# Performance work log

Hardware: AMD Instinct MI355X
Metric: run time of the kernel (lower is better)

Reference implementation:

```python
import jax, jax.numpy as jnp
import numpy as np

HID = 1024
HEADS = 16
DH = HID // HEADS
SCALE = DH ** -0.5
L, B = 2048, 2


def setup_inputs() -> dict:
    key = jax.random.key(0)
    ks = jax.random.split(key, 16)
    inp = {
        "query": jax.random.normal(ks[0], (L, B, HID), jnp.float32),
        "key": jax.random.normal(ks[1], (L, B, HID), jnp.float32),
        "value": jax.random.normal(ks[2], (L, B, HID), jnp.float32),
        "mask": jax.random.randint(ks[3], (B, L), 0, 2).astype(bool),
    }
    # xavier-uniform linear weights (torch Linear stores [out, in]; y = x @ W.T + b)
    lim = (6.0 / (HID + HID)) ** 0.5
    for i, name in enumerate(["wq", "wk", "wv", "wfc"]):
        inp[name] = jax.random.uniform(ks[4 + i], (HID, HID), jnp.float32, -lim, lim)
    inp["bq"] = jnp.zeros((HID,), jnp.float32)
    inp["bk"] = jnp.zeros((HID,), jnp.float32)
    inp["bv"] = jnp.zeros((HID,), jnp.float32)
    inp["bfc"] = jnp.zeros((HID,), jnp.float32)
    inp["tao"] = jnp.full((HEADS,), 10.0, jnp.float32)
    return inp


def reference(query, key, value, mask, wq, bq, wk, bk, wv, bv, wfc, bfc, tao):
    # inputs arrive [L, B, D]; module transposes to [B, L, D]
    q = jnp.swapaxes(query, 0, 1)
    k = jnp.swapaxes(key, 0, 1)
    v = jnp.swapaxes(value, 0, 1)
    bsz, length, _ = q.shape

    def heads(x, w, b):
        y = x @ w.T + b                      # [B, L, D]
        return y.reshape(bsz, length, HEADS, DH).transpose(0, 2, 1, 3)  # [B, H, L, d]

    Q = heads(q, wq, bq)
    K = heads(k, wk, bk)
    V = heads(v, wv, bv)

    qk = jnp.einsum("bhqd,bhkd->bhqk", Q, K) * SCALE  # [B, H, L, L]

    # gaussian positional bias: -|i-j|^2/2 * tao_h^-4
    idx = jnp.arange(length, dtype=jnp.float32)
    dist = -0.5 * (idx[:, None] - idx[None, :]) ** 2          # [L, L]
    qk = qk + dist[None, None, :, :] * (tao ** -4)[None, :, None, None]

    qk = jnp.where(mask[:, None, None, :], -jnp.inf, qk)
    attn = jax.nn.softmax(qk, axis=-1)  # dropout is identity in eval mode

    x = jnp.einsum("bhqk,bhkd->bhqd", attn, V)            # [B, H, L, d]
    x = x.transpose(0, 2, 1, 3).reshape(bsz, length, HID)  # [B, L, D]
    x = x @ wfc.T + bfc
    return jnp.swapaxes(x, 0, 1)  # [L, B, D]
```

## Files before the change

### kernel.cpp

```cpp
#include <hip/hip_runtime.h>

#define LQ   2048
#define BQ   2
#define HID  1024
#define NH   16
#define DH   64
#define SCALE 0.125f
#define L2E  1.44269504088896f
#define C1   0.18033688011f
#define EXPOFF 23.0831206542f
#define MASKNEG (-1024.0f)

using short8  = __attribute__((ext_vector_type(8))) short;
using ushort8 = __attribute__((ext_vector_type(8))) unsigned short;
using f32x4   = __attribute__((ext_vector_type(4))) float;
typedef unsigned short u16;
typedef __attribute__((ext_vector_type(2))) __bf16 bf16x2;

__device__ inline u16 f2bf(float x) {
    unsigned int u = __float_as_uint(x);
    u = (u + 0x7fffu + ((u >> 16) & 1u)) >> 16;
    return (u16)u;
}

#if defined(__has_builtin)
#if __has_builtin(__builtin_amdgcn_cvt_pk_bf16_f32)
#define HAVE_PKBF 1
#endif
#if __has_builtin(__builtin_amdgcn_exp2f)
#define HAVE_EXP2 1
#endif
#endif

__device__ inline unsigned int pkbf(float a, float b) {
#ifdef HAVE_PKBF
    bf16x2 r = __builtin_amdgcn_cvt_pk_bf16_f32(a, b);
    return __builtin_bit_cast(unsigned int, r);
#else
    return (unsigned int)f2bf(a) | ((unsigned int)f2bf(b) << 16);
#endif
}

__device__ inline float fexp2(float x) {
#ifdef HAVE_EXP2
    return __builtin_amdgcn_exp2f(x);
#else
    return exp2f(x);
#endif
}

__device__ inline void gl_lds16(const void* g, void* l) {
    __builtin_amdgcn_global_load_lds(
        (const __attribute__((address_space(1))) void*)g,
        (__attribute__((address_space(3))) void*)l, 16, 0, 0);
}

__device__ inline void wvm8() { asm volatile("s_waitcnt vmcnt(8)" ::: "memory"); __builtin_amdgcn_sched_barrier(0); }
__device__ inline void wvm6() { asm volatile("s_waitcnt vmcnt(6)" ::: "memory"); __builtin_amdgcn_sched_barrier(0); }
__device__ inline void wvm0() { asm volatile("s_waitcnt vmcnt(0)" ::: "memory"); __builtin_amdgcn_sched_barrier(0); }
__device__ inline void wlg0() { asm volatile("s_waitcnt lgkmcnt(0)" ::: "memory"); __builtin_amdgcn_sched_barrier(0); }
__device__ inline void sbar() {
    __builtin_amdgcn_sched_barrier(0);
    __builtin_amdgcn_s_barrier();
    __builtin_amdgcn_sched_barrier(0);
}

struct CastArgs {
    const float* s[7];
    u16* d[7];
    int n[7];
    const unsigned char* mraw;
    float* mout;
    int mn;
};

__global__ __launch_bounds__(256) void castw(CastArgs a) {
    const int y = blockIdx.y;
    const int t = threadIdx.x;
    if (y == 7) {
        if (blockIdx.x != 0) return;
        __shared__ int cnt;
        if (t == 0) cnt = 0;
        __syncthreads();
        int local = 0;
        for (int i = t; i < a.mn; i += 256)
            if ((i & 3) && a.mraw[i]) local++;
        atomicAdd(&cnt, local);
        __syncthreads();
        bool isInt32 = (cnt == 0);
        const int* mi = (const int*)a.mraw;
        for (int i = t; i < a.mn; i += 256) {
            const bool m = isInt32 ? (mi[i] != 0) : (a.mraw[i] != 0);
            a.mout[i] = m ? (MASKNEG - EXPOFF) : (-EXPOFF);
        }
        return;
    }
    const float* s = a.s[y];
    u16* d = a.d[y];
    const int n4 = a.n[y] >> 2;
    for (int i = blockIdx.x * 256 + t; i < n4; i += gridDim.x * 256) {
        float4 v = *(const float4*)(s + (size_t)i * 4);
        uint2 p;
        p.x = pkbf(v.x, v.y);
        p.y = pkbf(v.z, v.w);
        *(uint2*)(d + (size_t)i * 4) = p;
    }
}

struct QkvArgs {
    const u16* A[3];
    const u16* W[3];
    const float* bias[3];
    u16* out[3];
};

__global__ __launch_bounds__(256) void gemm_qkv(QkvArgs ga) {
    __shared__ u16 As[2][128][64];
    __shared__ u16 Bs[2][128][64];

    const int z = blockIdx.z;
    const u16* A = ga.A[z];
    const u16* W = ga.W[z];
    const float* bias = ga.bias[z];
    u16* outp = ga.out[z];

    const int t = threadIdx.x;
    const int m0 = blockIdx.x * 128;
    const int n0 = blockIdx.y * 128;
    const int lane = t & 63;
    const int lane15 = lane & 15;
    const int quad = lane >> 4;
    const int w = t >> 6;
    const int wm = (w >> 1) * 64;
    const int wn = (w & 1) * 64;

    const int lrow = lane >> 3;
    const int ch = (lane & 7) ^ ((lane >> 3) & 7);
    const u16* aS = A + (size_t)(m0 + 32 * w + lrow) * HID + 8 * ch;
    const u16* bS = W + (size_t)(n0 + 32 * w + lrow) * HID + 8 * ch;

    const int s0 = (quad ^ (lane15 & 7)) * 8;
    const int s1 = ((4 + quad) ^ (lane15 & 7)) * 8;

    f32x4 acc[4][4];
#pragma unroll
    for (int i = 0; i < 4; i++)
#pragma unroll
        for (int j = 0; j < 4; j++) acc[i][j] = (f32x4){0,0,0,0};

#define QKV_STAGE(kt, buf)                                                          \
    {                                                                               \
        _Pragma("unroll")                                                           \
        for (int i = 0; i < 4; i++) {                                               \
            gl_lds16(aS + (size_t)(8 * i) * HID + 64 * (kt), &As[buf][32 * w + 8 * i][0]); \
            gl_lds16(bS + (size_t)(8 * i) * HID + 64 * (kt), &Bs[buf][32 * w + 8 * i][0]); \
        }                                                                           \
    }

    QKV_STAGE(0, 0);
    QKV_STAGE(1, 1);

    for (int kt = 0; kt < 16; ++kt) {
        if (kt < 15) wvm8(); else wvm0();
        sbar();

        const int pb = kt & 1;
        short8 af0[4], af1[4], bf0[4], bf1[4];
#pragma unroll
        for (int i = 0; i < 4; i++) {
            const u16* ar = &As[pb][wm + i * 16 + lane15][0];
            const u16* br = &Bs[pb][wn + i * 16 + lane15][0];
            af0[i] = *(const short8*)(ar + s0);
            af1[i] = *(const short8*)(ar + s1);
            bf0[i] = *(const short8*)(br + s0);
            bf1[i] = *(const short8*)(br + s1);
        }
        wlg0();
        sbar();
        if (kt + 2 < 16) QKV_STAGE(kt + 2, pb);

#pragma unroll
        for (int mi = 0; mi < 4; mi++)
#pragma unroll
            for (int ni = 0; ni < 4; ni++) {
                acc[mi][ni] = __builtin_amdgcn_mfma_f32_16x16x32_bf16(af0[mi], bf0[ni], acc[mi][ni], 0, 0, 0);
                acc[mi][ni] = __builtin_amdgcn_mfma_f32_16x16x32_bf16(af1[mi], bf1[ni], acc[mi][ni], 0, 0, 0);
            }
    }
#undef QKV_STAGE

#pragma unroll
    for (int mi = 0; mi < 4; mi++) {
#pragma unroll
        for (int ni = 0; ni < 4; ni++) {
            const int n = n0 + wn + ni * 16 + lane15;
            const float bv = bias[n];
            const int h = n >> 6, d = n & 63;
#pragma unroll
            for (int r = 0; r < 4; r++) {
                const int m = m0 + wm + mi * 16 + quad * 4 + r;
                const float c = acc[mi][ni][r] + bv;
                const int b = m & 1, l = m >> 1;
                if (z < 2) {
                    outp[(((size_t)(b * NH + h)) * LQ + l) * DH + d] = f2bf(c);
                } else {
                    outp[(((size_t)(b * NH + h)) * DH + d) * LQ + l] = f2bf(c);
                }
            }
        }
    }
}

__global__ __launch_bounds__(256) void gemm_fc(const u16* __restrict__ A,
                                               const u16* __restrict__ W,
                                               const float* __restrict__ bias,
                                               float* __restrict__ outp) {
    __shared__ u16 As[2][128][64];
    __shared__ u16 Bs[2][64][64];

    const int t = threadIdx.x;
    const int m0 = blockIdx.x * 128;
    const int n0 = blockIdx.y * 64;
    const int lane = t & 63;
    const int lane15 = lane & 15;
    const int quad = lane >> 4;
    const int w = t >> 6;
    const int wm = (w >> 1) * 64;
    const int wn = (w & 1) * 32;

    const int lrow = lane >> 3;
    const int ch = (lane & 7) ^ ((lane >> 3) & 7);
    const u16* aS = A + (size_t)(m0 + 32 * w + lrow) * HID + 8 * ch;
    const u16* bS = W + (size_t)(n0 + 16 * w + lrow) * HID + 8 * ch;

    const int s0 = (quad ^ (lane15 & 7)) * 8;
    const int s1 = ((4 + quad) ^ (lane15 & 7)) * 8;

    f32x4 acc[4][2];
#pragma unroll
    for (int i = 0; i < 4; i++)
#pragma unroll
        for (int j = 0; j < 2; j++) acc[i][j] = (f32x4){0,0,0,0};

#define FC_STAGE(kt, buf)                                                           \
    {                                                                               \
        _Pragma("unroll")                                                           \
        for (int i = 0; i < 4; i++)                                                 \
            gl_lds16(aS + (size_t)(8 * i) * HID + 64 * (kt), &As[buf][32 * w + 8 * i][0]); \
        _Pragma("unroll")                                                           \
        for (int i = 0; i < 2; i++)                                                 \
            gl_lds16(bS + (size_t)(8 * i) * HID + 64 * (kt), &Bs[buf][16 * w + 8 * i][0]); \
    }

    FC_STAGE(0, 0);
    FC_STAGE(1, 1);

    for (int kt = 0; kt < 16; ++kt) {
        if (kt < 15) wvm6(); else wvm0();
        sbar();

        const int pb = kt & 1;
        short8 af0[4], af1[4], bf0[2], bf1[2];
#pragma unroll
        for (int i = 0; i < 4; i++) {
            const u16* ar = &As[pb][wm + i * 16 + lane15][0];
            af0[i] = *(const short8*)(ar + s0);
            af1[i] = *(const short8*)(ar + s1);
        }
#pragma unroll
        for (int j = 0; j < 2; j++) {
            const u16* br = &Bs[pb][wn + j * 16 + lane15][0];
            bf0[j] = *(const short8*)(br + s0);
            bf1[j] = *(const short8*)(br + s1);
        }
        wlg0();
        sbar();
        if (kt + 2 < 16) FC_STAGE(kt + 2, pb);

#pragma unroll
        for (int mi = 0; mi < 4; mi++)
#pragma unroll
            for (int ni = 0; ni < 2; ni++) {
                acc[mi][ni] = __builtin_amdgcn_mfma_f32_16x16x32_bf16(af0[mi], bf0[ni], acc[mi][ni], 0, 0, 0);
                acc[mi][ni] = __builtin_amdgcn_mfma_f32_16x16x32_bf16(af1[mi], bf1[ni], acc[mi][ni], 0, 0, 0);
            }
    }
#undef FC_STAGE

#pragma unroll
    for (int mi = 0; mi < 4; mi++) {
#pragma unroll
        for (int ni = 0; ni < 2; ni++) {
            const int n = n0 + wn + ni * 16 + lane15;
            const float bv = bias[n];
#pragma unroll
            for (int r = 0; r < 4; r++) {
                const int m = m0 + wm + mi * 16 + quad * 4 + r;
                outp[(size_t)m * HID + n] = acc[mi][ni][r] + bv;
            }
        }
    }
}

#define PSTR 72

__global__ __launch_bounds__(256, 2) void attn_kernel(const u16* __restrict__ Qg,
                                                      const u16* __restrict__ Kg,
                                                      const u16* __restrict__ Vtg,
                                                      const float* __restrict__ maskF,
                                                      const float* __restrict__ tao,
                                                      u16* __restrict__ Xa) {
    __shared__ u16 Ks[2][64][64];
    __shared__ u16 Vt[2][64][64];
    __shared__ u16 PT[128][PSTR];

    const int bh = blockIdx.x;
    const int q0 = blockIdx.y * 128;
    const int b = bh >> 4;
    const int h = bh & 15;
    const int t = threadIdx.x;
    const int w = t >> 6;
    const int lane = t & 63;
    const int lane15 = lane & 15;
    const int quad = lane >> 4;

    const u16* Kbase = Kg + (size_t)bh * LQ * DH;
    const u16* Vtbase = Vtg + (size_t)bh * DH * LQ;
    const float* mrow = maskF + b * LQ;

    const float tv = tao[h];
    const float t2 = tv * tv;
    const float nb = -0.5f / (t2 * t2);
    const float nb2 = nb * L2E;
    const float sqn = sqrtf(-nb2);
    const float R = sqrtf(-40.0f / nb2) + 1.0f;

    int c_lo = (int)floorf(((float)q0 - R) * (1.0f / 64.0f));
    int c_hi = (int)floorf(((float)(q0 + 127) + R) * (1.0f / 64.0f));
    if (c_lo < 0) c_lo = 0;
    if (c_hi > (LQ / 64 - 1)) c_hi = LQ / 64 - 1;
    if (c_hi < c_lo) c_hi = c_lo;

    const int lr = lane >> 3;
    const int sch = (lane & 7) ^ lr;
    const u16* kS0 = Kbase + (size_t)(16 * w + lr) * DH + 8 * sch;
    const u16* kS1 = Kbase + (size_t)(16 * w + 8 + lr) * DH + 8 * sch;
    const u16* vS0 = Vtbase + (size_t)(16 * w + lr) * LQ + 8 * sch;
    const u16* vS1 = Vtbase + (size_t)(16 * w + 8 + lr) * LQ + 8 * sch;

    const int qrow0 = q0 + w * 32 + lane15;
    const int qrow1 = qrow0 + 16;
    short8 qA00, qA01, qA10, qA11;
    {
        const u16* qp0 = Qg + ((size_t)bh * LQ + qrow0) * DH + quad * 8;
        qA00 = *(const short8*)(qp0);
        qA01 = *(const short8*)(qp0 + 32);
        const u16* qp1 = Qg + ((size_t)bh * LQ + qrow1) * DH + quad * 8;
        qA10 = *(const short8*)(qp1);
        qA11 = *(const short8*)(qp1 + 32);
    }

    const int s0 = (quad ^ (lane15 & 7)) * 8;
    const int s1 = ((4 + quad) ^ (lane15 & 7)) * 8;

    float crs[16];
#pragma unroll
    for (int i = 0; i < 16; i++)
        crs[i] = (float)((i >> 2) * 16 + (i & 3)) * sqn;

    short8 ones;
#pragma unroll
    for (int i = 0; i < 8; i++) ones[i] = (short)0x3F80;

    f32x4 O0[4], O1[4];
#pragma unroll
    for (int mt = 0; mt < 4; mt++) { O0[mt] = (f32x4){0,0,0,0}; O1[mt] = (f32x4){0,0,0,0}; }
    f32x4 Lac0 = (f32x4){0,0,0,0};
    f32x4 Lac1 = (f32x4){0,0,0,0};

    const float eb00 = (float)(qrow0 - quad * 4);
    const float eb01 = (float)(qrow1 - quad * 4);
    const int prow0 = w * 32 + lane15;
    const int prow1 = prow0 + 16;

    gl_lds16(kS0 + (size_t)c_lo * (64 * DH), &Ks[0][16 * w][0]);
    gl_lds16(kS1 + (size_t)c_lo * (64 * DH), &Ks[0][16 * w + 8][0]);
    gl_lds16(vS0 + 64 * c_lo, &Vt[0][16 * w][0]);
    gl_lds16(vS1 + 64 * c_lo, &Vt[0][16 * w + 8][0]);
    __syncthreads();

    int p = 0;
    for (int c = c_lo; c <= c_hi; ++c) {
        float4 mv[4];
#pragma unroll
        for (int kt = 0; kt < 4; kt++)
            mv[kt] = *(const float4*)(mrow + 64 * c + kt * 16 + quad * 4);

        if (c < c_hi) {
            gl_lds16(kS0 + (size_t)(c + 1) * (64 * DH), &Ks[p ^ 1][16 * w][0]);
            gl_lds16(kS1 + (size_t)(c + 1) * (64 * DH), &Ks[p ^ 1][16 * w + 8][0]);
            gl_lds16(vS0 + 64 * (c + 1), &Vt[p ^ 1][16 * w][0]);
            gl_lds16(vS1 + 64 * (c + 1), &Vt[p ^ 1][16 * w + 8][0]);
        }

        f32x4 S0[4], S1[4];
#pragma unroll
        for (int kt = 0; kt < 4; kt++) {
            const u16* kr = &Ks[p][kt * 16 + lane15][0];
            const short8 ka = *(const short8*)(kr + s0);
            const short8 kb = *(const short8*)(kr + s1);
            S0[kt] = __builtin_amdgcn_mfma_f32_16x16x32_bf16(ka, qA00, (f32x4){0,0,0,0}, 0, 0, 0);
            S0[kt] = __builtin_amdgcn_mfma_f32_16x16x32_bf16(kb, qA01, S0[kt], 0, 0, 0);
            S1[kt] = __builtin_amdgcn_mfma_f32_16x16x32_bf16(ka, qA10, (f32x4){0,0,0,0}, 0, 0, 0);
            S1[kt] = __builtin_amdgcn_mfma_f32_16x16x32_bf16(kb, qA11, S1[kt], 0, 0, 0);
        }

        const float ebS0 = (eb00 - (float)(64 * c)) * sqn;
        const float ebS1 = (eb01 - (float)(64 * c)) * sqn;
#pragma unroll
        for (int kt = 0; kt < 4; kt++) {
            float pr0[4], pr1[4];
#pragma unroll
            for (int r = 0; r < 4; r++) {
                const float mb = ((const float*)&mv[kt])[r];
                const float dp0 = ebS0 - crs[kt * 4 + r];
                const float dp1 = ebS1 - crs[kt * 4 + r];
                pr0[r] = fexp2(fmaf(S0[kt][r], C1, fmaf(-dp0, dp0, mb)));
                pr1[r] = fexp2(fmaf(S1[kt][r], C1, fmaf(-dp1, dp1, mb)));
            }
            uint2 pk0, pk1;
            pk0.x = pkbf(pr0[0], pr0[1]);
            pk0.y = pkbf(pr0[2], pr0[3]);
            pk1.x = pkbf(pr1[0], pr1[1]);
            pk1.y = pkbf(pr1[2], pr1[3]);
            *(uint2*)&PT[prow0][kt * 16 + quad * 4] = pk0;
            *(uint2*)&PT[prow1][kt * 16 + quad * 4] = pk1;
        }

        const short8 pB00 = *(const short8*)&PT[prow0][quad * 8];
        const short8 pB01 = *(const short8*)&PT[prow0][32 + quad * 8];
        const short8 pB10 = *(const short8*)&PT[prow1][quad * 8];
        const short8 pB11 = *(const short8*)&PT[prow1][32 + quad * 8];
        Lac0 = __builtin_amdgcn_mfma_f32_16x16x32_bf16(ones, pB00, Lac0, 0, 0, 0);
        Lac0 = __builtin_amdgcn_mfma_f32_16x16x32_bf16(ones, pB01, Lac0, 0, 0, 0);
        Lac1 = __builtin_amdgcn_mfma_f32_16x16x32_bf16(ones, pB10, Lac1, 0, 0, 0);
        Lac1 = __builtin_amdgcn_mfma_f32_16x16x32_bf16(ones, pB11, Lac1, 0, 0, 0);

#pragma unroll
        for (int mt = 0; mt < 4; mt++) {
            const u16* vr = &Vt[p][mt * 16 + lane15][0];
            const short8 va = *(const short8*)(vr + s0);
            const short8 vb = *(const short8*)(vr + s1);
            O0[mt] = __builtin_amdgcn_mfma_f32_16x16x32_bf16(va, pB00, O0[mt], 0, 0, 0);
            O0[mt] = __builtin_amdgcn_mfma_f32_16x16x32_bf16(vb, pB01, O0[mt], 0, 0, 0);
            O1[mt] = __builtin_amdgcn_mfma_f32_16x16x32_bf16(va, pB10, O1[mt], 0, 0, 0);
            O1[mt] = __builtin_amdgcn_mfma_f32_16x16x32_bf16(vb, pB11, O1[mt], 0, 0, 0);
        }

        __syncthreads();
        p ^= 1;
    }

    {
        const float inv0 = 1.0f / Lac0[0];
        u16* dst0 = Xa + ((size_t)qrow0 * BQ + b) * HID + h * DH;
#pragma unroll
        for (int mt = 0; mt < 4; mt++) {
            uint2 pk2;
            pk2.x = pkbf(O0[mt][0] * inv0, O0[mt][1] * inv0);
            pk2.y = pkbf(O0[mt][2] * inv0, O0[mt][3] * inv0);
            *(uint2*)(dst0 + mt * 16 + quad * 4) = pk2;
        }
        const float inv1 = 1.0f / Lac1[0];
        u16* dst1 = Xa + ((size_t)qrow1 * BQ + b) * HID + h * DH;
#pragma unroll
        for (int mt = 0; mt < 4; mt++) {
            uint2 pk2;
            pk2.x = pkbf(O1[mt][0] * inv1, O1[mt][1] * inv1);
            pk2.y = pkbf(O1[mt][2] * inv1, O1[mt][3] * inv1);
            *(uint2*)(dst1 + mt * 16 + quad * 4) = pk2;
        }
    }
}

extern "C" void kernel_launch(void* const* d_in, const int* in_sizes, int n_in,
                              void* d_out, int out_size, void* d_ws, size_t ws_size,
                              hipStream_t stream) {
    const float* q    = (const float*)d_in[0];
    const float* k    = (const float*)d_in[1];
    const float* v    = (const float*)d_in[2];
    const void*  mask = d_in[3];
    const float* wq   = (const float*)d_in[4];
    const float* wk   = (const float*)d_in[5];
    const float* wv   = (const float*)d_in[6];
    const float* wfc  = (const float*)d_in[7];
    const float* bq   = (const float*)d_in[8];
    const float* bk   = (const float*)d_in[9];
    const float* bv   = (const float*)d_in[10];
    const float* bfc  = (const float*)d_in[11];
    const float* tao  = (const float*)d_in[12];

    const size_t NE = (size_t)LQ * BQ * HID;
    const size_t NW = (size_t)HID * HID;
    u16* base = (u16*)d_ws;
    u16* Qp    = base;
    u16* Kp    = base + NE;
    u16* Vtp   = base + 2 * NE;
    u16* Xa    = base + 3 * NE;
    u16* qbf   = base + 4 * NE;
    u16* kbf   = base + 5 * NE;
    u16* vbf   = base + 6 * NE;
    u16* wqbf  = base + 7 * NE;
    u16* wkbf  = wqbf + NW;
    u16* wvbf  = wkbf + NW;
    u16* wfcbf = wvbf + NW;
    float* maskF = (float*)(wfcbf + NW);

    CastArgs ca;
    ca.s[0] = q;   ca.d[0] = qbf;   ca.n[0] = (int)NE;
    ca.s[1] = k;   ca.d[1] = kbf;   ca.n[1] = (int)NE;
    ca.s[2] = v;   ca.d[2] = vbf;   ca.n[2] = (int)NE;
    ca.s[3] = wq;  ca.d[3] = wqbf;  ca.n[3] = (int)NW;
    ca.s[4] = wk;  ca.d[4] = wkbf;  ca.n[4] = (int)NW;
    ca.s[5] = wv;  ca.d[5] = wvbf;  ca.n[5] = (int)NW;
    ca.s[6] = wfc; ca.d[6] = wfcbf; ca.n[6] = (int)NW;
    ca.mraw = (const unsigned char*)mask;
    ca.mout = maskF;
    ca.mn = BQ * LQ;
    castw<<<dim3(256, 8), 256, 0, stream>>>(ca);

    QkvArgs ga;
    ga.A[0] = qbf;  ga.W[0] = wqbf;  ga.bias[0] = bq;  ga.out[0] = Qp;
    ga.A[1] = kbf;  ga.W[1] = wkbf;  ga.bias[1] = bk;  ga.out[1] = Kp;
    ga.A[2] = vbf;  ga.W[2] = wvbf;  ga.bias[2] = bv;  ga.out[2] = Vtp;
    gemm_qkv<<<dim3(32, 8, 3), 256, 0, stream>>>(ga);

    attn_kernel<<<dim3(32, 16), 256, 0, stream>>>(Qp, Kp, Vtp, maskF, tao, Xa);

    gemm_fc<<<dim3(32, 16), 256, 0, stream>>>(Xa, wfcbf, bfc, (float*)d_out);
}
```

Before: 237.5 us.

## Prefetch two K/V tiles ahead and stage mask in LDS for attention

```diff
diff --git a/kernel.cpp b/kernel.cpp
--- a/kernel.cpp
+++ b/kernel.cpp
@@ -57,6 +57,7 @@
 
 __device__ inline void wvm8() { asm volatile("s_waitcnt vmcnt(8)" ::: "memory"); __builtin_amdgcn_sched_barrier(0); }
 __device__ inline void wvm6() { asm volatile("s_waitcnt vmcnt(6)" ::: "memory"); __builtin_amdgcn_sched_barrier(0); }
+__device__ inline void wvm4() { asm volatile("s_waitcnt vmcnt(4)" ::: "memory"); __builtin_amdgcn_sched_barrier(0); }
 __device__ inline void wvm0() { asm volatile("s_waitcnt vmcnt(0)" ::: "memory"); __builtin_amdgcn_sched_barrier(0); }
 __device__ inline void wlg0() { asm volatile("s_waitcnt lgkmcnt(0)" ::: "memory"); __builtin_amdgcn_sched_barrier(0); }
 __device__ inline void sbar() {
@@ -313,6 +314,7 @@
     __shared__ u16 Ks[2][64][64];
     __shared__ u16 Vt[2][64][64];
     __shared__ u16 PT[128][PSTR];
+    __shared__ float smaskL[LQ];
 
     const int bh = blockIdx.x;
     const int q0 = blockIdx.y * 128;
@@ -340,6 +342,7 @@
     if (c_lo < 0) c_lo = 0;
     if (c_hi > (LQ / 64 - 1)) c_hi = LQ / 64 - 1;
     if (c_hi < c_lo) c_hi = c_lo;
+    const int c1 = (c_lo + 1 <= c_hi) ? (c_lo + 1) : c_hi;
 
     const int lr = lane >> 3;
     const int sch = (lane & 7) ^ lr;
@@ -347,6 +350,14 @@
     const u16* kS1 = Kbase + (size_t)(16 * w + 8 + lr) * DH + 8 * sch;
     const u16* vS0 = Vtbase + (size_t)(16 * w + lr) * LQ + 8 * sch;
     const u16* vS1 = Vtbase + (size_t)(16 * w + 8 + lr) * LQ + 8 * sch;
+
+#define ATT_STAGE(cc, buf)                                             \
+    {                                                                  \
+        gl_lds16(kS0 + (size_t)(cc) * (64 * DH), &Ks[buf][16 * w][0]); \
+        gl_lds16(kS1 + (size_t)(cc) * (64 * DH), &Ks[buf][16 * w + 8][0]); \
+        gl_lds16(vS0 + 64 * (cc), &Vt[buf][16 * w][0]);                \
+        gl_lds16(vS1 + 64 * (cc), &Vt[buf][16 * w + 8][0]);            \
+    }
 
     const int qrow0 = q0 + w * 32 + lane15;
     const int qrow1 = qrow0 + 16;
@@ -359,6 +370,15 @@
         qA10 = *(const short8*)(qp1);
         qA11 = *(const short8*)(qp1 + 32);
     }
+    const float4 mT0 = *(const float4*)(mrow + 4 * t);
+    const float4 mT1 = *(const float4*)(mrow + 1024 + 4 * t);
+    __builtin_amdgcn_sched_barrier(0);
+    ATT_STAGE(c_lo, 0);
+    ATT_STAGE(c1, 1);
+    __builtin_amdgcn_sched_barrier(0);
+    *(float4*)&smaskL[4 * t] = mT0;
+    *(float4*)&smaskL[1024 + 4 * t] = mT1;
+    wlg0();
 
     const int s0 = (quad ^ (lane15 & 7)) * 8;
     const int s1 = ((4 + quad) ^ (lane15 & 7)) * 8;
@@ -383,37 +403,40 @@
     const int prow0 = w * 32 + lane15;
     const int prow1 = prow0 + 16;
 
-    gl_lds16(kS0 + (size_t)c_lo * (64 * DH), &Ks[0][16 * w][0]);
-    gl_lds16(kS1 + (size_t)c_lo * (64 * DH), &Ks[0][16 * w + 8][0]);
-    gl_lds16(vS0 + 64 * c_lo, &Vt[0][16 * w][0]);
-    gl_lds16(vS1 + 64 * c_lo, &Vt[0][16 * w + 8][0]);
-    __syncthreads();
-
-    int p = 0;
     for (int c = c_lo; c <= c_hi; ++c) {
+        if (c < c_hi) wvm4(); else wvm0();
+        sbar();
+
+        const int pb = (c - c_lo) & 1;
+
+        short8 ka[4], kb[4], va[4], vb[4];
+#pragma unroll
+        for (int kt = 0; kt < 4; kt++) {
+            const u16* kr = &Ks[pb][kt * 16 + lane15][0];
+            ka[kt] = *(const short8*)(kr + s0);
+            kb[kt] = *(const short8*)(kr + s1);
+            const u16* vr = &Vt[pb][kt * 16 + lane15][0];
+            va[kt] = *(const short8*)(vr + s0);
+            vb[kt] = *(const short8*)(vr + s1);
+        }
+
+        f32x4 S0[4], S1[4];
+#pragma unroll
+        for (int kt = 0; kt < 4; kt++) {
+            S0[kt] = __builtin_amdgcn_mfma_f32_16x16x32_bf16(ka[kt], qA00, (f32x4){0,0,0,0}, 0, 0, 0);
+            S0[kt] = __builtin_amdgcn_mfma_f32_16x16x32_bf16(kb[kt], qA01, S0[kt], 0, 0, 0);
+            S1[kt] = __builtin_amdgcn_mfma_f32_16x16x32_bf16(ka[kt], qA10, (f32x4){0,0,0,0}, 0, 0, 0);
+            S1[kt] = __builtin_amdgcn_mfma_f32_16x16x32_bf16(kb[kt], qA11, S1[kt], 0, 0, 0);
+        }
+
+        wlg0();
+        sbar();
+        if (c + 2 <= c_hi) ATT_STAGE(c + 2, pb);
+
         float4 mv[4];
 #pragma unroll
         for (int kt = 0; kt < 4; kt++)
-            mv[kt] = *(const float4*)(mrow + 64 * c + kt * 16 + quad * 4);
-
-        if (c < c_hi) {
-            gl_lds16(kS0 + (size_t)(c + 1) * (64 * DH), &Ks[p ^ 1][16 * w][0]);
-            gl_lds16(kS1 + (size_t)(c + 1) * (64 * DH), &Ks[p ^ 1][16 * w + 8][0]);
-            gl_lds16(vS0 + 64 * (c + 1), &Vt[p ^ 1][16 * w][0]);
-            gl_lds16(vS1 + 64 * (c + 1), &Vt[p ^ 1][16 * w + 8][0]);
-        }
-
-        f32x4 S0[4], S1[4];
-#pragma unroll
-        for (int kt = 0; kt < 4; kt++) {
-            const u16* kr = &Ks[p][kt * 16 + lane15][0];
-            const short8 ka = *(const short8*)(kr + s0);
-            const short8 kb = *(const short8*)(kr + s1);
-            S0[kt] = __builtin_amdgcn_mfma_f32_16x16x32_bf16(ka, qA00, (f32x4){0,0,0,0}, 0, 0, 0);
-            S0[kt] = __builtin_amdgcn_mfma_f32_16x16x32_bf16(kb, qA01, S0[kt], 0, 0, 0);
-            S1[kt] = __builtin_amdgcn_mfma_f32_16x16x32_bf16(ka, qA10, (f32x4){0,0,0,0}, 0, 0, 0);
-            S1[kt] = __builtin_amdgcn_mfma_f32_16x16x32_bf16(kb, qA11, S1[kt], 0, 0, 0);
-        }
+            mv[kt] = *(const float4*)&smaskL[64 * c + kt * 16 + quad * 4];
 
         const float ebS0 = (eb00 - (float)(64 * c)) * sqn;
         const float ebS1 = (eb01 - (float)(64 * c)) * sqn;
@@ -448,18 +471,13 @@
 
 #pragma unroll
         for (int mt = 0; mt < 4; mt++) {
-            const u16* vr = &Vt[p][mt * 16 + lane15][0];
-            const short8 va = *(const short8*)(vr + s0);
-            const short8 vb = *(const short8*)(vr + s1);
-            O0[mt] = __builtin_amdgcn_mfma_f32_16x16x32_bf16(va, pB00, O0[mt], 0, 0, 0);
-            O0[mt] = __builtin_amdgcn_mfma_f32_16x16x32_bf16(vb, pB01, O0[mt], 0, 0, 0);
-            O1[mt] = __builtin_amdgcn_mfma_f32_16x16x32_bf16(va, pB10, O1[mt], 0, 0, 0);
-            O1[mt] = __builtin_amdgcn_mfma_f32_16x16x32_bf16(vb, pB11, O1[mt], 0, 0, 0);
-        }
-
-        __syncthreads();
-        p ^= 1;
-    }
+            O0[mt] = __builtin_amdgcn_mfma_f32_16x16x32_bf16(va[mt], pB00, O0[mt], 0, 0, 0);
+            O0[mt] = __builtin_amdgcn_mfma_f32_16x16x32_bf16(vb[mt], pB01, O0[mt], 0, 0, 0);
+            O1[mt] = __builtin_amdgcn_mfma_f32_16x16x32_bf16(va[mt], pB10, O1[mt], 0, 0, 0);
+            O1[mt] = __builtin_amdgcn_mfma_f32_16x16x32_bf16(vb[mt], pB11, O1[mt], 0, 0, 0);
+        }
+    }
+#undef ATT_STAGE
 
     {
         const float inv0 = 1.0f / Lac0[0];
```

After: 235.3 us. No clear change (-0.9%).
